# Performance work log

Measured on AMD Instinct MI355X. Metric: run time of the kernel, lower is better.

Reference implementation:

```python
import jax, jax.numpy as jnp
import numpy as np

KER = 3          # CausalPool1d kernel
PAD_VAL = 1e-8   # left-pad value
K = 3            # harmonic_num
H = 4200         # rows of integral matrix
F = 321          # frequency bins


def setup_inputs() -> dict:
    key = jax.random.key(0)
    k1, k2, k3 = jax.random.split(key, 3)
    mag = jax.random.uniform(k1, (8, 2, F, 1000), dtype=jnp.float32)          # B,C,F,T (magnitude >= 0)
    integral_m = jax.random.normal(k2, (H, F), dtype=jnp.float32)             # buffer integral_m (squeezed)
    harmonic_loc = jax.random.normal(k3, (H, F), dtype=jnp.float32)           # buffer harmonic_loc (squeezed)
    return {"mag": mag, "integral_m": integral_m, "harmonic_loc": harmonic_loc, "freq_dim": F}


def reference(mag, integral_m, harmonic_loc, freq_dim):
    # harmonic_nominee: (B,C,H,T) = integral_m @ mag
    nominee = jnp.einsum('hf,bcft->bcht', integral_m, mag)
    # topk over the H axis (torch dim=-2); lax.top_k works on last axis -> move H last
    _, pos = jax.lax.top_k(jnp.moveaxis(nominee, 2, -1), K)  # (B,C,T,K), descending like torch
    pos = jnp.moveaxis(pos, -1, 2).astype(jnp.float32)       # (B,C,K,T)
    # CausalPool1d: left-pad (KER-1) with 1e-8, avg over window KER, stride 1 (vectorized over K)
    xp = jnp.pad(pos, ((0, 0), (0, 0), (0, 0), (KER - 1, 0)), constant_values=PAD_VAL)
    T = pos.shape[-1]
    choose = ((xp[..., 0:T] + xp[..., 1:T + 1] + xp[..., 2:T + 2]) / KER).astype(jnp.int32)  # (B,C,K,T)
    # gather harmonic_loc rows and accumulate over the K harmonics
    gathered = harmonic_loc[choose]          # (B,C,K,T,F)
    summed = gathered.sum(axis=2)            # (B,C,T,F)
    # (B,C,F,T) threshold mask, matching torch's (x > 0).float()
    out = (jnp.swapaxes(summed, -1, -2) > 0).astype(jnp.float32)
    return out
```

## Files before the change

### kernel.cpp

```cpp
#include <hip/hip_runtime.h>
#include <math.h>

#define F_DIM 321
#define H_DIM 4200
#define T_DIM 1000
#define NBC   16
#define KTOP  3
#define PADV  1e-8f

#define BM 32
#define BN 256
#define NRT 132
#define NG  80
#define NTT 4

typedef float v4f __attribute__((ext_vector_type(4)));

__device__ __forceinline__ void ins3(float v, int i,
                                     float& v0, float& v1, float& v2,
                                     int& i0, int& i1, int& i2) {
  if (v > v0)      { v2 = v1; i2 = i1; v1 = v0; i1 = i0; v0 = v; i0 = i; }
  else if (v > v1) { v2 = v1; i2 = i1; v1 = v;  i1 = i; }
  else if (v > v2) { v2 = v;  i2 = i; }
}

#define LOADB(B0, B1, B2, B3, g) do {                                  \
    const float* _p = pB + (size_t)((g) * 4) * T_DIM;                  \
    B0 = *(const v4f*)(_p);                                            \
    B1 = *(const v4f*)(_p + T_DIM);                                    \
    B2 = *(const v4f*)(_p + 2 * T_DIM);                                \
    B3 = *(const v4f*)(_p + 3 * T_DIM);                                \
  } while (0)

#define FMAG(B0, B1, B2, B3, g) do {                                   \
    float _a[8][4];                                                    \
    _Pragma("unroll") for (int r = 0; r < 8; ++r)                      \
      _Pragma("unroll") for (int q = 0; q < 4; ++q)                    \
        _a[r][q] = im[ab[r] + (g) * 4 + q];                            \
    _Pragma("unroll") for (int r = 0; r < 8; ++r)                      \
      _Pragma("unroll") for (int c = 0; c < 4; ++c) {                  \
        acc[r][c] = fmaf(_a[r][0], B0[c], acc[r][c]);                  \
        acc[r][c] = fmaf(_a[r][1], B1[c], acc[r][c]);                  \
        acc[r][c] = fmaf(_a[r][2], B2[c], acc[r][c]);                  \
        acc[r][c] = fmaf(_a[r][3], B3[c], acc[r][c]);                  \
      }                                                                \
  } while (0)

__global__ __launch_bounds__(256)
void hi_k1_gemm_top3(const float* __restrict__ mag,
                     const float* __restrict__ im,
                     float* __restrict__ wv, int* __restrict__ wi,
                     int nsplit) {
  const int tid  = threadIdx.x;
  const int lane = tid & 63;
  const int w    = tid >> 6;
  const int t0 = blockIdx.x * BN;
  const int bc = blockIdx.y;
  const int sp = blockIdx.z;
  const int rt_begin = (sp * NRT) / nsplit;
  const int rt_end   = ((sp + 1) * NRT) / nsplit;

  __shared__ float mv[4 * BN * KTOP];
  __shared__ int   mi[4 * BN * KTOP];

  const float* magbc = mag + (size_t)bc * F_DIM * T_DIM;
  const float* pB = magbc + t0 + lane * 4;

  float gv0 = -INFINITY, gv1 = -INFINITY, gv2 = -INFINITY;
  int   gi0 = 0, gi1 = 0, gi2 = 0;

  for (int rt = rt_begin; rt < rt_end; ++rt) {
    const int h0 = rt * BM;
    int ab[8];
#pragma unroll
    for (int r = 0; r < 8; ++r) {
      int gh = h0 + w * 8 + r;
      if (gh >= H_DIM) gh = H_DIM - 1;
      ab[r] = __builtin_amdgcn_readfirstlane(gh * F_DIM);
    }

    float acc[8][4];
#pragma unroll
    for (int r = 0; r < 8; ++r)
#pragma unroll
      for (int c = 0; c < 4; ++c) acc[r][c] = 0.f;

    v4f Bc0, Bc1, Bc2, Bc3, Bn0, Bn1, Bn2, Bn3;
    LOADB(Bc0, Bc1, Bc2, Bc3, 0);

#pragma unroll 1
    for (int gs = 0; gs < NG / 2; ++gs) {
      const int ge = 2 * gs, go = 2 * gs + 1;
      LOADB(Bn0, Bn1, Bn2, Bn3, go);
      FMAG(Bc0, Bc1, Bc2, Bc3, ge);
      if (ge + 2 < NG) LOADB(Bc0, Bc1, Bc2, Bc3, ge + 2);
      FMAG(Bn0, Bn1, Bn2, Bn3, go);
    }

    {
      float bt[4];
#pragma unroll
      for (int c = 0; c < 4; ++c) {
        int gt = t0 + lane * 4 + c;
        bt[c] = (gt < T_DIM) ? magbc[(size_t)(F_DIM - 1) * T_DIM + gt] : 0.f;
      }
#pragma unroll
      for (int r = 0; r < 8; ++r) {
        float av = im[ab[r] + (F_DIM - 1)];
#pragma unroll
        for (int c = 0; c < 4; ++c) acc[r][c] = fmaf(av, bt[c], acc[r][c]);
      }
    }

#pragma unroll
    for (int c = 0; c < 4; ++c) {
      const int col = lane * 4 + c;
      float v0 = -INFINITY, v1 = -INFINITY, v2 = -INFINITY;
      int   i0 = 0, i1 = 0, i2 = 0;
#pragma unroll
      for (int r = 0; r < 8; ++r) {
        int gh = h0 + w * 8 + r;
        float v = (gh < H_DIM) ? acc[r][c] : -INFINITY;
        ins3(v, gh, v0, v1, v2, i0, i1, i2);
      }
      mv[(w * BN + col) * 3 + 0] = v0;
      mv[(w * BN + col) * 3 + 1] = v1;
      mv[(w * BN + col) * 3 + 2] = v2;
      mi[(w * BN + col) * 3 + 0] = i0;
      mi[(w * BN + col) * 3 + 1] = i1;
      mi[(w * BN + col) * 3 + 2] = i2;
    }
    __syncthreads();
    {
      const int col = tid;
#pragma unroll
      for (int ww = 0; ww < 4; ++ww)
#pragma unroll
        for (int j = 0; j < 3; ++j) {
          float v = mv[(ww * BN + col) * 3 + j];
          int   i = mi[(ww * BN + col) * 3 + j];
          ins3(v, i, gv0, gv1, gv2, gi0, gi1, gi2);
        }
    }
    __syncthreads();
  }

  {
    int t = t0 + tid;
    if (t < T_DIM) {
      size_t base = ((size_t)(bc * nsplit + sp) * KTOP) * T_DIM + t;
      wv[base]             = gv0;
      wv[base + T_DIM]     = gv1;
      wv[base + 2 * T_DIM] = gv2;
      wi[base]             = gi0;
      wi[base + T_DIM]     = gi1;
      wi[base + 2 * T_DIM] = gi2;
    }
  }
}

__global__ __launch_bounds__(256, 4)
void hi_k3_pool_gather(const float* __restrict__ wv, const int* __restrict__ wi,
                       const float* __restrict__ hl, float* __restrict__ out,
                       int nsplit) {
  const int tid = threadIdx.x;
  const int t0 = blockIdx.x * 64;
  const int bc = blockIdx.y;

  __shared__ float pos_lds[66 * KTOP];
  __shared__ int   rows[64 * KTOP];
  __shared__ float S[64 * 65];

  if (tid < 66) {
    int t = t0 - 2 + tid;
    float p0 = PADV, p1 = PADV, p2 = PADV;
    if (t >= 0 && t < T_DIM) {
      float v0 = -INFINITY, v1 = -INFINITY, v2 = -INFINITY;
      int i0 = 0, i1 = 0, i2 = 0;
      for (int sp = 0; sp < nsplit; ++sp)
        for (int j = 0; j < KTOP; ++j) {
          size_t idx = ((size_t)(bc * nsplit + sp) * KTOP + j) * T_DIM + t;
          ins3(wv[idx], wi[idx], v0, v1, v2, i0, i1, i2);
        }
      p0 = (float)i0; p1 = (float)i1; p2 = (float)i2;
    }
    pos_lds[tid * KTOP + 0] = p0;
    pos_lds[tid * KTOP + 1] = p1;
    pos_lds[tid * KTOP + 2] = p2;
  }
  __syncthreads();
  if (tid < 64) {
#pragma unroll
    for (int k = 0; k < KTOP; ++k) {
      float s = (pos_lds[tid * KTOP + k] + pos_lds[(tid + 1) * KTOP + k])
                + pos_lds[(tid + 2) * KTOP + k];
      rows[tid * KTOP + k] = (int)(s / 3.0f);
    }
  }
  __syncthreads();

  const int w = tid >> 6, lane = tid & 63;
  for (int fc = 0; fc < 6; ++fc) {
    const int f0 = fc * 64;
    for (int i = 0; i < 16; ++i) {
      int tl = w * 16 + i;
      int r0 = rows[tl * KTOP + 0];
      int r1 = rows[tl * KTOP + 1];
      int r2 = rows[tl * KTOP + 2];
      int f = f0 + lane;
      float s = 0.f;
      if (f < F_DIM)
        s = (hl[(size_t)r0 * F_DIM + f] + hl[(size_t)r1 * F_DIM + f])
            + hl[(size_t)r2 * F_DIM + f];
      S[tl * 65 + lane] = s;
    }
    __syncthreads();
#pragma unroll
    for (int i = 0; i < 16; ++i) {
      int e = tid + 256 * i;
      int fl = e >> 6, tl = e & 63;
      int f = f0 + fl, t = t0 + tl;
      if (f < F_DIM && t < T_DIM)
        out[((size_t)bc * F_DIM + f) * T_DIM + t] = (S[tl * 65 + fl] > 0.f) ? 1.f : 0.f;
    }
    __syncthreads();
  }
}

extern "C" void kernel_launch(void* const* d_in, const int* in_sizes, int n_in,
                              void* d_out, int out_size, void* d_ws, size_t ws_size,
                              hipStream_t stream) {
  const float* mag = (const float*)d_in[0];
  const float* im  = (const float*)d_in[1];
  const float* hl  = (const float*)d_in[2];
  float* out = (float*)d_out;

  int nsplit = 8;
  if (ws_size >= (size_t)NBC * 32 * KTOP * T_DIM * 8) nsplit = 32;
  else if (ws_size >= (size_t)NBC * 16 * KTOP * T_DIM * 8) nsplit = 16;
  float* wv = (float*)d_ws;
  int*   wi = (int*)d_ws + (size_t)NBC * nsplit * KTOP * T_DIM;

  dim3 g1(NTT, NBC, nsplit);
  hipLaunchKernelGGL(hi_k1_gemm_top3, g1, dim3(256), 0, stream, mag, im, wv, wi, nsplit);

  dim3 g3((T_DIM + 63) / 64, NBC);
  hipLaunchKernelGGL(hi_k3_pool_gather, g3, dim3(256), 0, stream, wv, wi, hl, out, nsplit);
}
```

Measured before the change: 938.1 us.

## Stage integral rows in LDS and cover all time columns per block

The GEMM+top3 kernel now uses 512-thread blocks that span the whole time axis. Each thread computes 16 rows by 2 columns, and a 16-row slab of integral_m is staged in LDS instead of being read through wave-uniform scalar loads. This removes the per-tile cross-wave LDS merge and its extra barrier, because each thread keeps its own running top-3. The row-split count rises to 64 to restore parallelism. The trade-offs are more LDS reads per FMA, smaller per-thread B vectors, and more partial results for the gather kernel to merge.

```diff
diff --git a/kernel.cpp b/kernel.cpp
--- a/kernel.cpp
+++ b/kernel.cpp
@@ -8,13 +8,13 @@
 #define KTOP  3
 #define PADV  1e-8f
 
-#define BM 32
-#define BN 256
-#define NRT 132
+#define BM 16
+#define LDR 324
+#define NRT 263
 #define NG  80
-#define NTT 4
 
 typedef float v4f __attribute__((ext_vector_type(4)));
+typedef float v2f __attribute__((ext_vector_type(2)));
 
 __device__ __forceinline__ void ins3(float v, int i,
                                      float& v0, float& v1, float& v2,
@@ -26,66 +26,67 @@
 
 #define LOADB(B0, B1, B2, B3, g) do {                                  \
     const float* _p = pB + (size_t)((g) * 4) * T_DIM;                  \
-    B0 = *(const v4f*)(_p);                                            \
-    B1 = *(const v4f*)(_p + T_DIM);                                    \
-    B2 = *(const v4f*)(_p + 2 * T_DIM);                                \
-    B3 = *(const v4f*)(_p + 3 * T_DIM);                                \
+    B0 = *(const v2f*)(_p);                                            \
+    B1 = *(const v2f*)(_p + T_DIM);                                    \
+    B2 = *(const v2f*)(_p + 2 * T_DIM);                                \
+    B3 = *(const v2f*)(_p + 3 * T_DIM);                                \
   } while (0)
 
 #define FMAG(B0, B1, B2, B3, g) do {                                   \
-    float _a[8][4];                                                    \
-    _Pragma("unroll") for (int r = 0; r < 8; ++r)                      \
-      _Pragma("unroll") for (int q = 0; q < 4; ++q)                    \
-        _a[r][q] = im[ab[r] + (g) * 4 + q];                            \
-    _Pragma("unroll") for (int r = 0; r < 8; ++r)                      \
-      _Pragma("unroll") for (int c = 0; c < 4; ++c) {                  \
-        acc[r][c] = fmaf(_a[r][0], B0[c], acc[r][c]);                  \
-        acc[r][c] = fmaf(_a[r][1], B1[c], acc[r][c]);                  \
-        acc[r][c] = fmaf(_a[r][2], B2[c], acc[r][c]);                  \
-        acc[r][c] = fmaf(_a[r][3], B3[c], acc[r][c]);                  \
+    _Pragma("unroll") for (int r = 0; r < 16; ++r) {                   \
+      const v4f Ar = *(const v4f*)(&Alds[r * LDR + (g) * 4]);          \
+      _Pragma("unroll") for (int c = 0; c < 2; ++c) {                  \
+        acc[r][c] = fmaf(Ar[0], B0[c], acc[r][c]);                     \
+        acc[r][c] = fmaf(Ar[1], B1[c], acc[r][c]);                     \
+        acc[r][c] = fmaf(Ar[2], B2[c], acc[r][c]);                     \
+        acc[r][c] = fmaf(Ar[3], B3[c], acc[r][c]);                     \
       }                                                                \
+    }                                                                  \
   } while (0)
 
-__global__ __launch_bounds__(256)
+__global__ __launch_bounds__(512)
 void hi_k1_gemm_top3(const float* __restrict__ mag,
                      const float* __restrict__ im,
                      float* __restrict__ wv, int* __restrict__ wi,
                      int nsplit) {
   const int tid  = threadIdx.x;
   const int lane = tid & 63;
-  const int w    = tid >> 6;
-  const int t0 = blockIdx.x * BN;
+  const int tg   = tid >> 6;
   const int bc = blockIdx.y;
-  const int sp = blockIdx.z;
+  const int sp = blockIdx.x;
   const int rt_begin = (sp * NRT) / nsplit;
   const int rt_end   = ((sp + 1) * NRT) / nsplit;
-
-  __shared__ float mv[4 * BN * KTOP];
-  __shared__ int   mi[4 * BN * KTOP];
+  const int tcol0 = tg * 128 + lane * 2;
+
+  __shared__ __align__(16) float Alds[BM * LDR];
 
   const float* magbc = mag + (size_t)bc * F_DIM * T_DIM;
-  const float* pB = magbc + t0 + lane * 4;
-
-  float gv0 = -INFINITY, gv1 = -INFINITY, gv2 = -INFINITY;
-  int   gi0 = 0, gi1 = 0, gi2 = 0;
+  const float* pB = magbc + tcol0;
+
+  float gv[2][3], gi_f; int gi[2][3];
+#pragma unroll
+  for (int c = 0; c < 2; ++c)
+#pragma unroll
+    for (int j = 0; j < 3; ++j) { gv[c][j] = -INFINITY; gi[c][j] = 0; }
+  (void)gi_f;
 
   for (int rt = rt_begin; rt < rt_end; ++rt) {
     const int h0 = rt * BM;
-    int ab[8];
-#pragma unroll
-    for (int r = 0; r < 8; ++r) {
-      int gh = h0 + w * 8 + r;
+
+    {
+      const int r = tid >> 5, i0 = tid & 31;
+      int gh = h0 + r;
       if (gh >= H_DIM) gh = H_DIM - 1;
-      ab[r] = __builtin_amdgcn_readfirstlane(gh * F_DIM);
-    }
-
-    float acc[8][4];
-#pragma unroll
-    for (int r = 0; r < 8; ++r)
-#pragma unroll
-      for (int c = 0; c < 4; ++c) acc[r][c] = 0.f;
-
-    v4f Bc0, Bc1, Bc2, Bc3, Bn0, Bn1, Bn2, Bn3;
+      const float* srow = im + (size_t)gh * F_DIM;
+      for (int j = i0; j < F_DIM; j += 32) Alds[r * LDR + j] = srow[j];
+    }
+    __syncthreads();
+
+    float acc[16][2];
+#pragma unroll
+    for (int r = 0; r < 16; ++r) { acc[r][0] = 0.f; acc[r][1] = 0.f; }
+
+    v2f Bc0, Bc1, Bc2, Bc3, Bn0, Bn1, Bn2, Bn3;
     LOADB(Bc0, Bc1, Bc2, Bc3, 0);
 
 #pragma unroll 1
@@ -98,63 +99,48 @@
     }
 
     {
-      float bt[4];
-#pragma unroll
-      for (int c = 0; c < 4; ++c) {
-        int gt = t0 + lane * 4 + c;
+      float bt[2];
+#pragma unroll
+      for (int c = 0; c < 2; ++c) {
+        int gt = tcol0 + c;
         bt[c] = (gt < T_DIM) ? magbc[(size_t)(F_DIM - 1) * T_DIM + gt] : 0.f;
       }
 #pragma unroll
-      for (int r = 0; r < 8; ++r) {
-        float av = im[ab[r] + (F_DIM - 1)];
-#pragma unroll
-        for (int c = 0; c < 4; ++c) acc[r][c] = fmaf(av, bt[c], acc[r][c]);
+      for (int r = 0; r < 16; ++r) {
+        float av = Alds[r * LDR + (F_DIM - 1)];
+        acc[r][0] = fmaf(av, bt[0], acc[r][0]);
+        acc[r][1] = fmaf(av, bt[1], acc[r][1]);
       }
     }
 
 #pragma unroll
-    for (int c = 0; c < 4; ++c) {
-      const int col = lane * 4 + c;
+    for (int c = 0; c < 2; ++c) {
       float v0 = -INFINITY, v1 = -INFINITY, v2 = -INFINITY;
       int   i0 = 0, i1 = 0, i2 = 0;
 #pragma unroll
-      for (int r = 0; r < 8; ++r) {
-        int gh = h0 + w * 8 + r;
+      for (int r = 0; r < 16; ++r) {
+        int gh = h0 + r;
         float v = (gh < H_DIM) ? acc[r][c] : -INFINITY;
         ins3(v, gh, v0, v1, v2, i0, i1, i2);
       }
-      mv[(w * BN + col) * 3 + 0] = v0;
-      mv[(w * BN + col) * 3 + 1] = v1;
-      mv[(w * BN + col) * 3 + 2] = v2;
-      mi[(w * BN + col) * 3 + 0] = i0;
-      mi[(w * BN + col) * 3 + 1] = i1;
-      mi[(w * BN + col) * 3 + 2] = i2;
-    }
-    __syncthreads();
-    {
-      const int col = tid;
-#pragma unroll
-      for (int ww = 0; ww < 4; ++ww)
-#pragma unroll
-        for (int j = 0; j < 3; ++j) {
-          float v = mv[(ww * BN + col) * 3 + j];
-          int   i = mi[(ww * BN + col) * 3 + j];
-          ins3(v, i, gv0, gv1, gv2, gi0, gi1, gi2);
-        }
-    }
-    __syncthreads();
-  }
-
-  {
-    int t = t0 + tid;
+      ins3(v0, i0, gv[c][0], gv[c][1], gv[c][2], gi[c][0], gi[c][1], gi[c][2]);
+      ins3(v1, i1, gv[c][0], gv[c][1], gv[c][2], gi[c][0], gi[c][1], gi[c][2]);
+      ins3(v2, i2, gv[c][0], gv[c][1], gv[c][2], gi[c][0], gi[c][1], gi[c][2]);
+    }
+    __syncthreads();
+  }
+
+#pragma unroll
+  for (int c = 0; c < 2; ++c) {
+    int t = tcol0 + c;
     if (t < T_DIM) {
       size_t base = ((size_t)(bc * nsplit + sp) * KTOP) * T_DIM + t;
-      wv[base]             = gv0;
-      wv[base + T_DIM]     = gv1;
-      wv[base + 2 * T_DIM] = gv2;
-      wi[base]             = gi0;
-      wi[base + T_DIM]     = gi1;
-      wi[base + 2 * T_DIM] = gi2;
+      wv[base]             = gv[c][0];
+      wv[base + T_DIM]     = gv[c][1];
+      wv[base + 2 * T_DIM] = gv[c][2];
+      wi[base]             = gi[c][0];
+      wi[base + T_DIM]     = gi[c][1];
+      wi[base + 2 * T_DIM] = gi[c][2];
     }
   }
 }
@@ -235,14 +221,14 @@
   const float* hl  = (const float*)d_in[2];
   float* out = (float*)d_out;
 
-  int nsplit = 8;
-  if (ws_size >= (size_t)NBC * 32 * KTOP * T_DIM * 8) nsplit = 32;
-  else if (ws_size >= (size_t)NBC * 16 * KTOP * T_DIM * 8) nsplit = 16;
+  int nsplit = 16;
+  if (ws_size >= (size_t)NBC * 64 * KTOP * T_DIM * 8) nsplit = 64;
+  else if (ws_size >= (size_t)NBC * 32 * KTOP * T_DIM * 8) nsplit = 32;
   float* wv = (float*)d_ws;
   int*   wi = (int*)d_ws + (size_t)NBC * nsplit * KTOP * T_DIM;
 
-  dim3 g1(NTT, NBC, nsplit);
-  hipLaunchKernelGGL(hi_k1_gemm_top3, g1, dim3(256), 0, stream, mag, im, wv, wi, nsplit);
+  dim3 g1(nsplit, NBC);
+  hipLaunchKernelGGL(hi_k1_gemm_top3, g1, dim3(512), 0, stream, mag, im, wv, wi, nsplit);
 
   dim3 g3((T_DIM + 63) / 64, NBC);
   hipLaunchKernelGGL(hi_k3_pool_gather, g3, dim3(256), 0, stream, wv, wi, hl, out, nsplit);
```

Measured after the change: 1.382 ms. 47.3% more time.
